# Kernel optimization log

Measured on AMD Instinct MI355X. Metric: run time of the kernel, lower is better.

The kernel has to match this reference:

```python
import jax, jax.numpy as jnp
import numpy as np

N_NODES = 50000
N_EDGES = 800000
IN_CH = 512
HID = 128
OUT_CH = 2
N_GRAPHS = 64
EPS = 1e-5


def _gcn_conv(x, src, dst, W, b):
    # GCNConv: out = D^-1/2 (A + I) D^-1/2 (x W) + b  (PyG semantics, self-loops added)
    n = x.shape[0]
    h = x @ W  # [N, H]
    loop = jnp.arange(n)
    src2 = jnp.concatenate([src, loop])
    dst2 = jnp.concatenate([dst, loop])
    deg = jax.ops.segment_sum(jnp.ones_like(dst2, dtype=h.dtype), dst2, num_segments=n)
    dinv = jax.lax.rsqrt(deg)  # deg >= 1 due to self-loops
    norm = dinv[src2] * dinv[dst2]  # [E+N]
    msg = h[src2] * norm[:, None]  # gather + normalize
    out = jax.ops.segment_sum(msg, dst2, num_segments=n)  # scatter-add
    return out + b


def _batchnorm_eval(x, gamma, beta, rm, rv):
    return (x - rm) * jax.lax.rsqrt(rv + EPS) * gamma + beta


def setup_inputs() -> dict:
    key = jax.random.key(0)
    ks = jax.random.split(key, 16)
    x = jax.random.normal(ks[0], (N_NODES, IN_CH), dtype=jnp.float32)
    edge_index = jax.random.randint(ks[1], (2, N_EDGES), 0, N_NODES, dtype=jnp.int64)
    batch = jnp.sort(jax.random.randint(ks[2], (N_NODES,), 0, N_GRAPHS, dtype=jnp.int64))
    s1 = 1.0 / np.sqrt(IN_CH)
    s2 = 1.0 / np.sqrt(HID)
    return {
        'x': x,
        'edge_index': edge_index,
        'batch': batch,
        'W1': jax.random.normal(ks[3], (IN_CH, HID), dtype=jnp.float32) * s1,
        'b1': jnp.zeros((HID,), dtype=jnp.float32),
        'gamma1': jax.random.normal(ks[4], (HID,), dtype=jnp.float32) * 0.1 + 1.0,
        'beta1': jax.random.normal(ks[5], (HID,), dtype=jnp.float32) * 0.1,
        'rm1': jax.random.normal(ks[6], (HID,), dtype=jnp.float32) * 0.1,
        'rv1': jax.random.uniform(ks[7], (HID,), dtype=jnp.float32, minval=0.5, maxval=1.5),
        'W2': jax.random.normal(ks[8], (HID, HID), dtype=jnp.float32) * s2,
        'b2': jnp.zeros((HID,), dtype=jnp.float32),
        'gamma2': jax.random.normal(ks[9], (HID,), dtype=jnp.float32) * 0.1 + 1.0,
        'beta2': jax.random.normal(ks[10], (HID,), dtype=jnp.float32) * 0.1,
        'rm2': jax.random.normal(ks[11], (HID,), dtype=jnp.float32) * 0.1,
        'rv2': jax.random.uniform(ks[12], (HID,), dtype=jnp.float32, minval=0.5, maxval=1.5),
        'Wl': jax.random.normal(ks[13], (HID, OUT_CH), dtype=jnp.float32) * s2,
        'bl': jnp.zeros((OUT_CH,), dtype=jnp.float32),
    }


def reference(x, edge_index, batch, W1, b1, gamma1, beta1, rm1, rv1,
              W2, b2, gamma2, beta2, rm2, rv2, Wl, bl):
    # Eval mode: BatchNorm uses running stats; dropout is identity.
    src, dst = edge_index[0], edge_index[1]
    h = _gcn_conv(x, src, dst, W1, b1)
    h = jax.nn.relu(_batchnorm_eval(h, gamma1, beta1, rm1, rv1))
    h = _gcn_conv(h, src, dst, W2, b2)
    h = jax.nn.relu(_batchnorm_eval(h, gamma2, beta2, rm2, rv2))
    # global mean pool over graphs in the batch
    sums = jax.ops.segment_sum(h, batch, num_segments=N_GRAPHS)  # [G, H]
    counts = jax.ops.segment_sum(jnp.ones((h.shape[0],), dtype=h.dtype), batch, num_segments=N_GRAPHS)
    pooled = sums / jnp.maximum(counts, 1.0)[:, None]
    return pooled @ Wl + bl  # [G, OUT_CH]
```

## Files before the change

kernel.cpp:

```cpp
#include <hip/hip_runtime.h>

#define EPSV 1e-5f

typedef __attribute__((ext_vector_type(8))) short short8;
typedef __attribute__((ext_vector_type(4))) float f32x4;
typedef unsigned int uint;
typedef unsigned short ushort;

__global__ __launch_bounds__(256) void init_k(int* __restrict__ cnt, int nnodes) {
    int i = blockIdx.x * 256 + threadIdx.x;
    if (i < nnodes) cnt[i] = 0;
}

__global__ __launch_bounds__(128) void gstart_k(const int* __restrict__ batch,
                                                int* __restrict__ gstart,
                                                int nnodes, int ngraphs) {
    int g = threadIdx.x;
    if (g > ngraphs) return;
    int lo = 0, hi = nnodes;
    while (lo < hi) {
        int mid = (lo + hi) >> 1;
        if (batch[mid] < g) lo = mid + 1; else hi = mid;
    }
    gstart[g] = lo;
}

__global__ __launch_bounds__(256) void degcount_k(const int* __restrict__ dst,
                                                  int* __restrict__ cnt,
                                                  int nedges) {
    int i = blockIdx.x * 256 + threadIdx.x;
    if (i < nedges) atomicAdd(&cnt[dst[i]], 1);
}

__global__ __launch_bounds__(256) void dinv_k(const int* __restrict__ cnt,
                                              float* __restrict__ dinv, int nnodes) {
    int i = blockIdx.x * 256 + threadIdx.x;
    if (i < nnodes) dinv[i] = rsqrtf(1.0f + (float)cnt[i]);
}

__global__ __launch_bounds__(256) void scan1_k(const int* __restrict__ cnt,
                                               int* __restrict__ rowptr,
                                               int* __restrict__ bsum, int n) {
    __shared__ int sh[256];
    const int tx = threadIdx.x;
    const int base = blockIdx.x * 1024;
    int v[4];
    int s = 0;
#pragma unroll
    for (int j = 0; j < 4; j++) {
        int idx = base + tx * 4 + j;
        v[j] = (idx < n) ? cnt[idx] : 0;
        s += v[j];
    }
    sh[tx] = s;
    __syncthreads();
#pragma unroll
    for (int off = 1; off < 256; off <<= 1) {
        int t = (tx >= off) ? sh[tx - off] : 0;
        __syncthreads();
        sh[tx] += t;
        __syncthreads();
    }
    int run = sh[tx] - s;
#pragma unroll
    for (int j = 0; j < 4; j++) {
        int idx = base + tx * 4 + j;
        if (idx < n) rowptr[idx] = run;
        run += v[j];
    }
    if (tx == 255) bsum[blockIdx.x] = sh[255];
}

__global__ __launch_bounds__(64) void scan2_k(int* __restrict__ bsum, int nb) {
    __shared__ int sh[64];
    const int tx = threadIdx.x;
    int v = (tx < nb) ? bsum[tx] : 0;
    sh[tx] = v;
    __syncthreads();
#pragma unroll
    for (int off = 1; off < 64; off <<= 1) {
        int t = (tx >= off) ? sh[tx - off] : 0;
        __syncthreads();
        sh[tx] += t;
        __syncthreads();
    }
    if (tx < nb) bsum[tx] = sh[tx] - v;
}

__global__ __launch_bounds__(256) void scan3_k(int* __restrict__ rowptr,
                                               int* __restrict__ cur,
                                               const int* __restrict__ bsum,
                                               int n, int nedges) {
    const int tx = threadIdx.x;
    const int base = blockIdx.x * 1024;
    int off = bsum[blockIdx.x];
#pragma unroll
    for (int j = 0; j < 4; j++) {
        int idx = base + tx * 4 + j;
        if (idx < n) {
            int r = rowptr[idx] + off;
            rowptr[idx] = r;
            cur[idx] = r;
        }
    }
    if (blockIdx.x == 0 && tx == 0) rowptr[n] = nedges;
}

__global__ __launch_bounds__(256) void fill_k(const int* __restrict__ src,
                                              const int* __restrict__ dst,
                                              int* __restrict__ cur,
                                              int* __restrict__ esrc, int nedges) {
    int i = blockIdx.x * 256 + threadIdx.x;
    if (i >= nedges) return;
    int pos = atomicAdd(&cur[dst[i]], 1);
    esrc[pos] = src[i];
}

template <int K>
__global__ __launch_bounds__(256) void wprep_k(const float* __restrict__ W,
                                               ushort* __restrict__ wThi,
                                               ushort* __restrict__ wTlo) {
    int i = blockIdx.x * 256 + threadIdx.x;
    if (i >= K * 128) return;
    int k = i >> 7, c = i & 127;
    float x = W[i];
    unsigned u = __builtin_bit_cast(unsigned, x);
    ushort hi = (ushort)(u >> 16);
    float hif = __builtin_bit_cast(float, u & 0xffff0000u);
    float lof = x - hif;
    ushort lo = (ushort)(__builtin_bit_cast(unsigned, lof) >> 16);
    wThi[c * K + k] = hi;
    wTlo[c * K + k] = lo;
}

template <int K>
__global__ __launch_bounds__(256) void gemm_mfma_k(const float* __restrict__ X,
                                                   const ushort* __restrict__ wThi,
                                                   const ushort* __restrict__ wTlo,
                                                   const float* __restrict__ dinv,
                                                   float* __restrict__ H,
                                                   ushort* __restrict__ hb16,
                                                   int nrows) {
    __shared__ ushort bsm[2][8192];

    const int tx = threadIdx.x;
    const int wu = __builtin_amdgcn_readfirstlane(tx >> 6);
    const int l = tx & 63;
    const int lrow = l & 15;
    const int kgrp = l >> 4;
    const int row0 = blockIdx.x * 64 + wu * 16;

    const ushort* sp[4];
#pragma unroll
    for (int q = 0; q < 4; q++) {
        int chunk = (wu * 4 + q) * 64 + l;
        int c = chunk >> 3;
        int sl = (chunk & 7) ^ (c & 7);
        sp[q] = ((sl >> 2) ? wTlo : wThi) + (size_t)c * K + (sl & 3) * 8;
    }

    int arow = row0 + lrow;
    if (arow >= nrows) arow = nrows - 1;
    const float* xrow = X + (size_t)arow * K + kgrp * 8;

    f32x4 acc[8];
#pragma unroll
    for (int g = 0; g < 8; g++) acc[g] = (f32x4){0.f, 0.f, 0.f, 0.f};

    auto STAGE = [&](int buf, int k0) {
#pragma unroll
        for (int q = 0; q < 4; q++) {
            const ushort* src = sp[q] + k0;
            ushort* dst = &bsm[buf][(wu * 4 + q) * 512];
            __builtin_amdgcn_global_load_lds(
                (const __attribute__((address_space(1))) unsigned int*)(const void*)src,
                (__attribute__((address_space(3))) unsigned int*)(void*)dst,
                16, 0, 0);
        }
    };

    constexpr int NIT = K / 32;
    STAGE(0, 0);
    f32x4 xa = *reinterpret_cast<const f32x4*>(xrow);
    f32x4 xb = *reinterpret_cast<const f32x4*>(xrow + 4);
    __syncthreads();

    for (int i = 0; i < NIT; i++) {
        const int cur = i & 1;
        if (i + 1 < NIT) STAGE(cur ^ 1, (i + 1) * 32);
        f32x4 na = xa, nb = xb;
        if (i + 1 < NIT) {
            na = *reinterpret_cast<const f32x4*>(xrow + (i + 1) * 32);
            nb = *reinterpret_cast<const f32x4*>(xrow + (i + 1) * 32 + 4);
        }

        short8 ah, al;
#pragma unroll
        for (int j = 0; j < 8; j++) {
            float f = (j < 4) ? xa[j] : xb[j - 4];
            unsigned u = __builtin_bit_cast(unsigned, f);
            ah[j] = (short)(u >> 16);
            float hif = __builtin_bit_cast(float, u & 0xffff0000u);
            float lof = f - hif;
            al[j] = (short)(__builtin_bit_cast(unsigned, lof) >> 16);
        }

        const ushort* b = bsm[cur];
#pragma unroll
        for (int g = 0; g < 8; g++) {
            int c = g * 16 + lrow;
            int sw = c & 7;
            short8 bh = *reinterpret_cast<const short8*>(&b[c * 64 + ((kgrp ^ sw) * 8)]);
            short8 bl = *reinterpret_cast<const short8*>(&b[c * 64 + (((4 | kgrp) ^ sw) * 8)]);
            acc[g] = __builtin_amdgcn_mfma_f32_16x16x32_bf16(ah, bh, acc[g], 0, 0, 0);
            acc[g] = __builtin_amdgcn_mfma_f32_16x16x32_bf16(al, bh, acc[g], 0, 0, 0);
            acc[g] = __builtin_amdgcn_mfma_f32_16x16x32_bf16(ah, bl, acc[g], 0, 0, 0);
        }
        __syncthreads();
        xa = na; xb = nb;
    }

#pragma unroll
    for (int r = 0; r < 4; r++) {
        int row = row0 + kgrp * 4 + r;
        if (row < nrows) {
            float dn = dinv[row];
            float* hrow = H + (size_t)row * 128 + lrow;
            ushort* hbrow = hb16 + (size_t)row * 128 + lrow;
#pragma unroll
            for (int g = 0; g < 8; g++) {
                float v = acc[g][r];
                hrow[g * 16] = v;
                unsigned u = __builtin_bit_cast(unsigned, v * dn);
                hbrow[g * 16] = (ushort)((u + 0x7fffu + ((u >> 16) & 1u)) >> 16);
            }
        }
    }
}

__global__ __launch_bounds__(256) void agg_k(const float* __restrict__ H,
                                             const uint* __restrict__ hb,
                                             const int* __restrict__ rowptr,
                                             const int* __restrict__ esrc,
                                             const float* __restrict__ dinv,
                                             const float* __restrict__ bias,
                                             const float* __restrict__ gamma,
                                             const float* __restrict__ beta,
                                             const float* __restrict__ rm,
                                             const float* __restrict__ rv,
                                             float* __restrict__ OUT,
                                             int nnodes) {
    int node = blockIdx.x * 4 + (threadIdx.x >> 6);
    if (node >= nnodes) return;
    node = __builtin_amdgcn_readfirstlane(node);
    const int l = threadIdx.x & 63;
    const int c = l * 2;
    const float dn = dinv[node];
    const int beg = rowptr[node], end = rowptr[node + 1];

    float2 hv = *reinterpret_cast<const float2*>(H + (size_t)node * 128 + c);
    float ax0 = hv.x * dn, ay0 = hv.y * dn;
    float ax1 = 0.f, ay1 = 0.f, ax2 = 0.f, ay2 = 0.f, ax3 = 0.f, ay3 = 0.f;
    const uint* hbl = hb + l;

    int j = beg;
    for (; j + 3 < end; j += 4) {
        int s0 = esrc[j], s1 = esrc[j + 1], s2 = esrc[j + 2], s3 = esrc[j + 3];
        uint u0 = hbl[(size_t)s0 * 64];
        uint u1 = hbl[(size_t)s1 * 64];
        uint u2 = hbl[(size_t)s2 * 64];
        uint u3 = hbl[(size_t)s3 * 64];
        ax0 += __builtin_bit_cast(float, u0 << 16);
        ay0 += __builtin_bit_cast(float, u0 & 0xffff0000u);
        ax1 += __builtin_bit_cast(float, u1 << 16);
        ay1 += __builtin_bit_cast(float, u1 & 0xffff0000u);
        ax2 += __builtin_bit_cast(float, u2 << 16);
        ay2 += __builtin_bit_cast(float, u2 & 0xffff0000u);
        ax3 += __builtin_bit_cast(float, u3 << 16);
        ay3 += __builtin_bit_cast(float, u3 & 0xffff0000u);
    }
    for (; j < end; j++) {
        uint u0 = hbl[(size_t)esrc[j] * 64];
        ax0 += __builtin_bit_cast(float, u0 << 16);
        ay0 += __builtin_bit_cast(float, u0 & 0xffff0000u);
    }
    float accx = (ax0 + ax1) + (ax2 + ax3);
    float accy = (ay0 + ay1) + (ay2 + ay3);

    float v0 = accx * dn + bias[c];
    float v1 = accy * dn + bias[c + 1];
    v0 = (v0 - rm[c])     * rsqrtf(rv[c] + EPSV)     * gamma[c]     + beta[c];
    v1 = (v1 - rm[c + 1]) * rsqrtf(rv[c + 1] + EPSV) * gamma[c + 1] + beta[c + 1];
    v0 = fmaxf(v0, 0.0f);
    v1 = fmaxf(v1, 0.0f);

    *reinterpret_cast<float2*>(OUT + (size_t)node * 128 + c) = make_float2(v0, v1);
}

__global__ __launch_bounds__(256) void pool1_k(const float* __restrict__ V,
                                               const int* __restrict__ gstart,
                                               float* __restrict__ partial) {
    __shared__ float sh[256];
    const int g = blockIdx.x >> 5;
    const int p = blockIdx.x & 31;
    const int tx = threadIdx.x;
    const int ch = tx & 127;
    const int sub = tx >> 7;
    const int beg = gstart[g], end = gstart[g + 1];
    const int chunk = (end - beg + 31) >> 5;
    const int s = beg + p * chunk;
    const int e = min(s + chunk, end);
    float acc = 0.0f;
    for (int i = s + sub; i < e; i += 2)
        acc += V[(size_t)i * 128 + ch];
    sh[tx] = acc;
    __syncthreads();
    if (tx < 128)
        partial[(size_t)blockIdx.x * 128 + tx] = sh[tx] + sh[tx + 128];
}

__global__ __launch_bounds__(128) void pool2_k(const float* __restrict__ partial,
                                               const int* __restrict__ gstart,
                                               float* __restrict__ pooled) {
    const int g = blockIdx.x;
    const int ch = threadIdx.x;
    float s = 0.0f;
#pragma unroll
    for (int p = 0; p < 32; p++)
        s += partial[(size_t)((g << 5) + p) * 128 + ch];
    float cnt = fmaxf((float)(gstart[g + 1] - gstart[g]), 1.0f);
    pooled[g * 128 + ch] = s / cnt;
}

__global__ __launch_bounds__(128) void final_k(const float* __restrict__ pooled,
                                               const float* __restrict__ Wl,
                                               const float* __restrict__ bl,
                                               float* __restrict__ out) {
    int tx = threadIdx.x;
    int g = tx >> 1, o = tx & 1;
    float s = 0.0f;
#pragma unroll 8
    for (int c = 0; c < 128; c++) s += pooled[g * 128 + c] * Wl[c * 2 + o];
    out[tx] = s + bl[o];
}

extern "C" void kernel_launch(void* const* d_in, const int* in_sizes, int n_in,
                              void* d_out, int out_size, void* d_ws, size_t ws_size,
                              hipStream_t stream) {
    const float* x      = (const float*)d_in[0];
    const int*   ei     = (const int*)d_in[1];
    const int*   batch  = (const int*)d_in[2];
    const float* W1     = (const float*)d_in[3];
    const float* b1     = (const float*)d_in[4];
    const float* gamma1 = (const float*)d_in[5];
    const float* beta1  = (const float*)d_in[6];
    const float* rm1    = (const float*)d_in[7];
    const float* rv1    = (const float*)d_in[8];
    const float* W2     = (const float*)d_in[9];
    const float* b2     = (const float*)d_in[10];
    const float* gamma2 = (const float*)d_in[11];
    const float* beta2  = (const float*)d_in[12];
    const float* rm2    = (const float*)d_in[13];
    const float* rv2    = (const float*)d_in[14];
    const float* Wl     = (const float*)d_in[15];
    const float* bl     = (const float*)d_in[16];
    float* out = (float*)d_out;

    const int nnodes  = in_sizes[2];
    const int nedges  = in_sizes[1] / 2;
    const int ngraphs = 64;
    const int* srcp = ei;
    const int* dstp = ei + nedges;

    float* wsA     = (float*)d_ws;
    float* wsB     = wsA + (size_t)nnodes * 128;
    float* dinv    = wsB + (size_t)nnodes * 128;
    float* pooled  = dinv + nnodes;
    float* partial = pooled + 64 * 128;
    int*   cnt     = (int*)(partial + 64 * 32 * 128);
    int*   rowptr  = cnt + nnodes;
    int*   cur     = rowptr + nnodes + 1;
    int*   bsum    = cur + nnodes;
    int*   gstart  = bsum + 64;
    int*   esrc    = gstart + 65;
    uintptr_t wp   = ((uintptr_t)(esrc + nedges) + 15) & ~(uintptr_t)15;
    ushort* wt1hi = (ushort*)wp;
    ushort* wt1lo = wt1hi + 512 * 128;
    ushort* wt2hi = wt1lo + 512 * 128;
    ushort* wt2lo = wt2hi + 128 * 128;
    ushort* hb16  = (ushort*)(wt2lo + 128 * 128);
    uint*   hb    = (uint*)hb16;

    dim3 blk(256);
    const int gNodes = (nnodes + 255) / 256;
    const int gEdges = (nedges + 255) / 256;
    const int gGemm  = (nnodes + 63) / 64;
    const int gAgg   = (nnodes + 3) / 4;
    const int nScanB = (nnodes + 1023) / 1024;

    init_k<<<gNodes, blk, 0, stream>>>(cnt, nnodes);
    gstart_k<<<1, 128, 0, stream>>>(batch, gstart, nnodes, ngraphs);
    wprep_k<512><<<(512 * 128) / 256, blk, 0, stream>>>(W1, wt1hi, wt1lo);
    wprep_k<128><<<(128 * 128) / 256, blk, 0, stream>>>(W2, wt2hi, wt2lo);
    degcount_k<<<gEdges, blk, 0, stream>>>(dstp, cnt, nedges);
    dinv_k<<<gNodes, blk, 0, stream>>>(cnt, dinv, nnodes);
    scan1_k<<<nScanB, blk, 0, stream>>>(cnt, rowptr, bsum, nnodes);
    scan2_k<<<1, 64, 0, stream>>>(bsum, nScanB);
    scan3_k<<<nScanB, blk, 0, stream>>>(rowptr, cur, bsum, nnodes, nedges);
    fill_k<<<gEdges, blk, 0, stream>>>(srcp, dstp, cur, esrc, nedges);

    gemm_mfma_k<512><<<gGemm, blk, 0, stream>>>(x, wt1hi, wt1lo, dinv, wsA, hb16, nnodes);
    agg_k<<<gAgg, blk, 0, stream>>>(wsA, hb, rowptr, esrc, dinv, b1, gamma1, beta1,
                                    rm1, rv1, wsB, nnodes);

    gemm_mfma_k<128><<<gGemm, blk, 0, stream>>>(wsB, wt2hi, wt2lo, dinv, wsA, hb16, nnodes);
    agg_k<<<gAgg, blk, 0, stream>>>(wsA, hb, rowptr, esrc, dinv, b2, gamma2, beta2,
                                    rm2, rv2, wsB, nnodes);

    pool1_k<<<ngraphs * 32, blk, 0, stream>>>(wsB, gstart, partial);
    pool2_k<<<ngraphs, 128, 0, stream>>>(partial, gstart, pooled);
    final_k<<<1, 128, 0, stream>>>(pooled, Wl, bl, out);
}
```

Baseline: 280.3 us.

## Triple-buffer weight tiles in GEMM with explicit vmcnt waits and prefetch depth two

```diff
diff --git a/kernel.cpp b/kernel.cpp
--- a/kernel.cpp
+++ b/kernel.cpp
@@ -141,7 +141,7 @@
                                                    float* __restrict__ H,
                                                    ushort* __restrict__ hb16,
                                                    int nrows) {
-    __shared__ ushort bsm[2][8192];
+    __shared__ ushort bsm[3][8192];
 
     const int tx = threadIdx.x;
     const int wu = __builtin_amdgcn_readfirstlane(tx >> 6);
@@ -180,24 +180,32 @@
     };
 
     constexpr int NIT = K / 32;
+
     STAGE(0, 0);
-    f32x4 xa = *reinterpret_cast<const f32x4*>(xrow);
-    f32x4 xb = *reinterpret_cast<const f32x4*>(xrow + 4);
-    __syncthreads();
-
+    STAGE(1, 32);
+    asm volatile("" ::: "memory");
+    f32x4 a0x = *reinterpret_cast<const f32x4*>(xrow);
+    f32x4 a0y = *reinterpret_cast<const f32x4*>(xrow + 4);
+    f32x4 a1x = *reinterpret_cast<const f32x4*>(xrow + 32);
+    f32x4 a1y = *reinterpret_cast<const f32x4*>(xrow + 36);
+
+#pragma unroll
     for (int i = 0; i < NIT; i++) {
-        const int cur = i & 1;
-        if (i + 1 < NIT) STAGE(cur ^ 1, (i + 1) * 32);
-        f32x4 na = xa, nb = xb;
-        if (i + 1 < NIT) {
-            na = *reinterpret_cast<const f32x4*>(xrow + (i + 1) * 32);
-            nb = *reinterpret_cast<const f32x4*>(xrow + (i + 1) * 32 + 4);
+        if (i + 1 < NIT) asm volatile("s_waitcnt vmcnt(6)" ::: "memory");
+        else             asm volatile("s_waitcnt vmcnt(0)" ::: "memory");
+        __builtin_amdgcn_s_barrier();
+        __builtin_amdgcn_sched_barrier(0);
+
+        f32x4 a2x = a1x, a2y = a1y;
+        if (i + 2 < NIT) {
+            a2x = *reinterpret_cast<const f32x4*>(xrow + (i + 2) * 32);
+            a2y = *reinterpret_cast<const f32x4*>(xrow + (i + 2) * 32 + 4);
         }
 
         short8 ah, al;
 #pragma unroll
         for (int j = 0; j < 8; j++) {
-            float f = (j < 4) ? xa[j] : xb[j - 4];
+            float f = (j < 4) ? a0x[j] : a0y[j - 4];
             unsigned u = __builtin_bit_cast(unsigned, f);
             ah[j] = (short)(u >> 16);
             float hif = __builtin_bit_cast(float, u & 0xffff0000u);
@@ -205,7 +213,7 @@
             al[j] = (short)(__builtin_bit_cast(unsigned, lof) >> 16);
         }
 
-        const ushort* b = bsm[cur];
+        const ushort* b = bsm[i % 3];
 #pragma unroll
         for (int g = 0; g < 8; g++) {
             int c = g * 16 + lrow;
@@ -216,8 +224,13 @@
             acc[g] = __builtin_amdgcn_mfma_f32_16x16x32_bf16(al, bh, acc[g], 0, 0, 0);
             acc[g] = __builtin_amdgcn_mfma_f32_16x16x32_bf16(ah, bl, acc[g], 0, 0, 0);
         }
-        __syncthreads();
-        xa = na; xb = nb;
+
+        asm volatile("" ::: "memory");
+        if (i + 2 < NIT) STAGE((i + 2) % 3, (i + 2) * 32);
+        asm volatile("" ::: "memory");
+
+        a0x = a1x; a0y = a1y;
+        a1x = a2x; a1y = a2y;
     }
 
 #pragma unroll
```

After: 276.1 us. Within noise of the previous version (-1.5%).
